# Kernel tuning notes

Hardware: AMD Instinct MI355X
Metric: run time of the kernel (lower is better)

## Reference

```python
import jax, jax.numpy as jnp
import numpy as np

B, N, DIM = 8, 2048, 512
HEADS, DIM_HEAD = 8, 64
INNER = HEADS * DIM_HEAD  # 512
SCALE = DIM_HEAD ** -0.5
NEG = -1e9


def setup_inputs() -> dict:
    key = jax.random.key(0)
    ks = jax.random.split(key, 7)
    x = jax.random.normal(ks[0], (B, N, DIM), dtype=jnp.float32)
    adj = jax.random.uniform(ks[1], (B, N, N), dtype=jnp.float32)
    att_mask = jax.random.randint(ks[2], (B, 1, N, N), 0, 2).astype(jnp.bool_)
    W_gcn = jax.random.normal(ks[3], (DIM, DIM), dtype=jnp.float32) * (DIM ** -0.5)
    W_qkv = jax.random.normal(ks[4], (DIM, 3 * INNER), dtype=jnp.float32) * (DIM ** -0.5)
    W_out = jax.random.normal(ks[5], (INNER + DIM, DIM), dtype=jnp.float32) * ((INNER + DIM) ** -0.5)
    b_out = jax.random.normal(ks[6], (DIM,), dtype=jnp.float32) * 0.01
    return {"x": x, "adj": adj, "att_mask": att_mask,
            "W_gcn": W_gcn, "W_qkv": W_qkv, "W_out": W_out, "b_out": b_out}


def reference(x, adj, att_mask, W_gcn, W_qkv, W_out, b_out):
    # GCN branch: adj @ (x W_gcn)  -> [b, n, dim]
    gcn = jnp.einsum('bnj,bjd->bnd', adj, x @ W_gcn)

    # Attention branch
    qkv = x @ W_qkv                                  # [b, n, 3*inner]
    q, k, v = jnp.split(qkv, 3, axis=-1)
    split_heads = lambda t: t.reshape(B, N, HEADS, DIM_HEAD).transpose(0, 2, 1, 3)
    q, k, v = split_heads(q), split_heads(k), split_heads(v)  # [b, h, n, d]

    dots = jnp.einsum('bhid,bhjd->bhij', q, k) * SCALE        # [b, h, n, n]
    dots = jnp.where(att_mask, NEG, dots)
    attn = jax.nn.softmax(dots, axis=-1)
    att_out = jnp.einsum('bhij,bhjd->bhid', attn, v)          # [b, h, n, d]
    att_out = att_out.transpose(0, 2, 1, 3).reshape(B, N, INNER)

    out = jnp.concatenate([att_out, gcn], axis=-1)            # [b, n, inner+dim]
    return out @ W_out + b_out                                # [b, n, dim]
```

## Files before the change

### kernel.cpp

```cpp
#include <hip/hip_runtime.h>
#include <stdint.h>

#define DEVFN __device__ __forceinline__

typedef __attribute__((ext_vector_type(8))) short short8;
typedef __attribute__((ext_vector_type(4))) short short4v;
typedef __attribute__((ext_vector_type(4))) float floatx4;
typedef __attribute__((ext_vector_type(16))) float floatx16;
typedef __attribute__((ext_vector_type(4))) float vfloat4;
typedef __attribute__((ext_vector_type(2))) unsigned int uint2v;
typedef __attribute__((ext_vector_type(4))) unsigned int uint4v;

#define MFMA_BF16(a,b,c) __builtin_amdgcn_mfma_f32_16x16x32_bf16((a),(b),(c),0,0,0)
#define MFMA32_BF16(a,b,c) __builtin_amdgcn_mfma_f32_32x32x16_bf16((a),(b),(c),0,0,0)
#define GL2LDS(g,l) __builtin_amdgcn_global_load_lds((const __attribute__((address_space(1))) void*)(g), (__attribute__((address_space(3))) void*)(l), 16, 0, 0)

DEVFN unsigned short f2bf(float f){
  unsigned u = __float_as_uint(f);
  u = (u + 0x7fffu + ((u >> 16) & 1u)) >> 16;
  return (unsigned short)u;
}

DEVFN unsigned cvtpk_bf16(float lo, float hi){
  unsigned r;
  asm("v_cvt_pk_bf16_f32 %0, %1, %2" : "=v"(r) : "v"(lo), "v"(hi));
  return r;
}

__global__ void detect_kernel(const unsigned char* m, unsigned int* flag){
  if (threadIdx.x == 0) *flag = 0u;
  __syncthreads();
  int any = 0;
  for (int i = threadIdx.x; i < 4096; i += 256)
    if ((i & 3) != 0 && m[i]) any = 1;
  if (any) atomicOr(flag, 1u);
}

__global__ void prep_kernel(const float* __restrict__ x, const float* __restrict__ wg,
                            const float* __restrict__ wq, const float* __restrict__ wo,
                            const void* __restrict__ mask, const unsigned* __restrict__ flag,
                            const float* __restrict__ adj,
                            unsigned short* __restrict__ xbf, unsigned short* __restrict__ wcat,
                            unsigned short* __restrict__ woutT, unsigned* __restrict__ mp,
                            unsigned short* __restrict__ adjb)
{
  int bid = blockIdx.x, tid = threadIdx.x;
  if (bid < 8192) {
    int i = (bid*256 + tid)*4;
    vfloat4 v = *(const vfloat4*)&x[i];
    short4v c; c[0]=(short)f2bf(v[0]); c[1]=(short)f2bf(v[1]); c[2]=(short)f2bf(v[2]); c[3]=(short)f2bf(v[3]);
    *(short4v*)&xbf[i] = c;
  } else if (bid < 8192 + 4096) {
    int i = (bid - 8192)*256 + tid;
    int k = i & 511, c = i >> 9;
    float v = (c < 512) ? wg[k*512 + c] : wq[k*1536 + (c - 512)];
    if (c >= 512 && c < 1024) v *= 0.18033688f;
    wcat[c*512 + k] = (unsigned short)f2bf(v);
  } else if (bid < 8192 + 4096 + 2048) {
    int i = (bid - 12288)*256 + tid;
    int k = i & 1023, n2 = i >> 10;
    woutT[n2*1024 + k] = (unsigned short)f2bf(wo[k*512 + n2]);
  } else if (bid < 145408) {
    int j = bid - 14336;
    int e = j*256 + tid;
    int v;
    if (*flag) v = ((const unsigned char*)mask)[e];
    else       v = ((const int*)mask)[e];
    unsigned long long ball = __ballot(v != 0);
    int base = e & ~63;
    int lane = tid & 63;
    if (lane == 0)  mp[(base >> 5) + 0] = (unsigned)(ball & 0xffffffffull);
    if (lane == 32) mp[(base >> 5) + 1] = (unsigned)(ball >> 32);
  } else {
    int i = ((bid - 145408)*256 + tid)*4;
    vfloat4 v = *(const vfloat4*)&adj[i];
    short4v c; c[0]=(short)f2bf(v[0]); c[1]=(short)f2bf(v[1]); c[2]=(short)f2bf(v[2]); c[3]=(short)f2bf(v[3]);
    *(short4v*)&adjb[i] = c;
  }
}

DEVFN void gemm_kloop_bf16(const unsigned short* Ag, int lda,
                           const unsigned short* Bg, int ldb, int K,
                           short* As, short* Bs, int w, int l,
                           floatx4 (&acc)[4][4])
{
  const int wr = (w >> 1)*64, wc = (w & 1)*64;
  for (int k0 = 0; k0 < K; k0 += 32) {
    __syncthreads();
#pragma unroll
    for (int i = 0; i < 2; i++) {
      int id = (w*2 + i)*64 + l;
      int row = id >> 2, part = id & 3;
      GL2LDS(Ag + row*lda + k0 + part*8, As + (w*2 + i)*512);
      GL2LDS(Bg + row*ldb + k0 + part*8, Bs + (w*2 + i)*512);
    }
    __syncthreads();
    short8 af[4], bfr[4];
#pragma unroll
    for (int t = 0; t < 4; t++) {
      af[t]  = *(const short8*)&As[(wr + t*16 + (l & 15))*32 + ((l >> 4) << 3)];
      bfr[t] = *(const short8*)&Bs[(wc + t*16 + (l & 15))*32 + ((l >> 4) << 3)];
    }
#pragma unroll
    for (int a2 = 0; a2 < 4; a2++)
#pragma unroll
      for (int b2 = 0; b2 < 4; b2++)
        acc[a2][b2] = MFMA_BF16(af[a2], bfr[b2], acc[a2][b2]);
  }
}

__global__ __launch_bounds__(256, 2)
void gemm_ab_kernel(const unsigned short* __restrict__ xbf, const unsigned short* __restrict__ wcat,
                    unsigned short* __restrict__ xgT, unsigned short* __restrict__ Qo,
                    unsigned short* __restrict__ Ko, unsigned short* __restrict__ VTo)
{
  __shared__ short lds[16384];
  int tid = threadIdx.x, w = tid >> 6, l = tid & 63;
  int bid = blockIdx.x;
  int xcd = bid & 7, slot = bid >> 3;
  int p  = xcd + ((slot >> 4) << 3);
  int nt = slot & 15;
  int rows0 = p*128, cols0 = nt*128;

  floatx4 acc[4][4];
  const floatx4 zf = {0.f, 0.f, 0.f, 0.f};
#pragma unroll
  for (int a2 = 0; a2 < 4; a2++)
#pragma unroll
    for (int b2 = 0; b2 < 4; b2++) acc[a2][b2] = zf;

  gemm_kloop_bf16(xbf + rows0*512, 512, wcat + cols0*512, 512, 512,
                  lds, lds + 4096, w, l, acc);
  __syncthreads();

  int wr = (w >> 1)*64, wc = (w & 1)*64;
  int b = p >> 4;
  int n0 = (p & 15)*128 + wr;
  int gc0 = cols0 + wc;

  if (nt < 4 || nt >= 12) {
    short* T = lds + w*4096;
#pragma unroll
    for (int mi = 0; mi < 4; mi++)
#pragma unroll
      for (int bi = 0; bi < 4; bi++)
#pragma unroll
        for (int r = 0; r < 4; r++) {
          int rl = mi*16 + ((l >> 4) << 2) + r;
          int cl = bi*16 + (l & 15);
          T[cl*64 + ((((rl >> 3) ^ (cl & 7))) << 3) + (rl & 7)] = (short)f2bf(acc[mi][bi][r]);
        }
#pragma unroll
    for (int i = 0; i < 8; i++) {
      int chunk = i*64 + l;
      int c = chunk >> 3, s = chunk & 7;
      short8 v = *(const short8*)&T[c*64 + ((s ^ (c & 7)) << 3)];
      int rowstart = n0 + s*8;
      if (nt < 4) {
        int d = gc0 + c;
        *(short8*)&xgT[(b*512 + d)*2048 + rowstart] = v;
      } else {
        int vc = gc0 + c - 1536;
        int hh = vc >> 6, dd = vc & 63;
        *(short8*)&VTo[((b*8 + hh)*64 + dd)*2048 + rowstart] = v;
      }
    }
  } else {
    unsigned short* dst = (nt < 8) ? Qo : Ko;
    int cbase = gc0 - ((nt < 8) ? 512 : 1024);
    int hh = cbase >> 6;
#pragma unroll
    for (int mi = 0; mi < 4; mi++)
#pragma unroll
      for (int bi = 0; bi < 4; bi++)
#pragma unroll
        for (int r = 0; r < 4; r++) {
          int rowg = n0 + mi*16 + ((l >> 4) << 2) + r;
          int dd = bi*16 + (l & 15);
          dst[((b*8 + hh)*2048 + rowg)*64 + dd] = (unsigned short)f2bf(acc[mi][bi][r]);
        }
  }
}

__global__ __launch_bounds__(256, 2)
void gemm_c_bf16_kernel(const unsigned short* __restrict__ adjb, const unsigned short* __restrict__ xgT,
                        unsigned short* __restrict__ cat)
{
  __shared__ short lds[8192];
  int tid = threadIdx.x, w = tid >> 6, l = tid & 63;
  int bid = blockIdx.x;
  int xcd = bid & 7, slot = bid >> 3;
  int p  = xcd + ((slot >> 2) << 3);
  int nt = slot & 3;
  int b = p >> 4, mt = p & 15;
  int rows0 = mt*128, cols0 = nt*128;

  floatx4 acc[4][4];
  const floatx4 zf = {0.f, 0.f, 0.f, 0.f};
#pragma unroll
  for (int a2 = 0; a2 < 4; a2++)
#pragma unroll
    for (int b2 = 0; b2 < 4; b2++) acc[a2][b2] = zf;

  gemm_kloop_bf16(adjb + (size_t)b*2048*2048 + (size_t)rows0*2048, 2048,
                  xgT + (b*512 + cols0)*2048, 2048, 2048,
                  lds, lds + 4096, w, l, acc);

  int wr = (w >> 1)*64, wc = (w & 1)*64;
#pragma unroll
  for (int mi = 0; mi < 4; mi++)
#pragma unroll
    for (int bi = 0; bi < 4; bi++)
#pragma unroll
      for (int r = 0; r < 4; r++) {
        int rowg = b*2048 + rows0 + wr + mi*16 + ((l >> 4) << 2) + r;
        int col  = 512 + cols0 + wc + bi*16 + (l & 15);
        cat[rowg*1024 + col] = (unsigned short)f2bf(acc[mi][bi][r]);
      }
}

__global__ __launch_bounds__(256, 2)
void gemm_c_f32_kernel(const float* __restrict__ adj, const unsigned short* __restrict__ xgT,
                       unsigned short* __restrict__ cat)
{
  __shared__ short lds[8192];
  int tid = threadIdx.x, w = tid >> 6, l = tid & 63;
  int bid = blockIdx.x;
  int xcd = bid & 7, slot = bid >> 3;
  int p  = xcd + ((slot >> 2) << 3);
  int nt = slot & 3;
  int b = p >> 4, mt = p & 15;
  int rows0 = mt*128, cols0 = nt*128;
  const float* Ag = adj + (size_t)b*2048*2048 + (size_t)rows0*2048;
  const unsigned short* Bg = xgT + (b*512 + cols0)*2048;

  floatx4 acc[4][4];
  const floatx4 zf = {0.f, 0.f, 0.f, 0.f};
#pragma unroll
  for (int a2 = 0; a2 < 4; a2++)
#pragma unroll
    for (int b2 = 0; b2 < 4; b2++) acc[a2][b2] = zf;

  const int wr = (w >> 1)*64, wc = (w & 1)*64;
  for (int k0 = 0; k0 < 2048; k0 += 32) {
    __syncthreads();
#pragma unroll
    for (int i = 0; i < 4; i++) {
      int id = (w*4 + i)*64 + l;
      int row = id >> 3, part = id & 7;
      vfloat4 v = *(const vfloat4*)&Ag[row*2048 + k0 + part*4];
      short4v c4; c4[0]=(short)f2bf(v[0]); c4[1]=(short)f2bf(v[1]); c4[2]=(short)f2bf(v[2]); c4[3]=(short)f2bf(v[3]);
      *(short4v*)&lds[row*32 + part*4] = c4;
    }
#pragma unroll
    for (int i = 0; i < 2; i++) {
      int id = (w*2 + i)*64 + l;
      int row = id >> 2, part = id & 3;
      GL2LDS(Bg + row*2048 + k0 + part*8, lds + 4096 + (w*2 + i)*512);
    }
    __syncthreads();
    short8 af[4], bfr[4];
#pragma unroll
    for (int t = 0; t < 4; t++) {
      af[t]  = *(const short8*)&lds[(wr + t*16 + (l & 15))*32 + ((l >> 4) << 3)];
      bfr[t] = *(const short8*)&lds[4096 + (wc + t*16 + (l & 15))*32 + ((l >> 4) << 3)];
    }
#pragma unroll
    for (int a2 = 0; a2 < 4; a2++)
#pragma unroll
      for (int b2 = 0; b2 < 4; b2++)
        acc[a2][b2] = MFMA_BF16(af[a2], bfr[b2], acc[a2][b2]);
  }

#pragma unroll
  for (int mi = 0; mi < 4; mi++)
#pragma unroll
    for (int bi = 0; bi < 4; bi++)
#pragma unroll
      for (int r = 0; r < 4; r++) {
        int rowg = b*2048 + rows0 + wr + mi*16 + ((l >> 4) << 2) + r;
        int col  = 512 + cols0 + wc + bi*16 + (l & 15);
        cat[rowg*1024 + col] = (unsigned short)f2bf(acc[mi][bi][r]);
      }
}

DEVFN void attn_stage(const unsigned short* KB, const unsigned short* VB,
                      short* Ks, short* Vs, int kn0, int w, int l)
{
#pragma unroll
  for (int i = 0; i < 2; i++) {
    int id = (w*2 + i)*64 + l;
    int row = id >> 3, sl = id & 7;
    int sp = sl ^ (row & 7) ^ (((row >> 3) & 3) << 1);
    GL2LDS(KB + (kn0 + row)*64 + sp*8, Ks + (w*2 + i)*512);
    GL2LDS(VB + row*2048 + kn0 + sp*8, Vs + (w*2 + i)*512);
  }
}

__global__ __launch_bounds__(256, 4)
void attn_kernel(const unsigned short* __restrict__ Q, const unsigned short* __restrict__ Kb,
                 const unsigned short* __restrict__ VT, const unsigned* __restrict__ mp,
                 unsigned short* __restrict__ cat)
{
  __shared__ short lds[16384];
  int tid = threadIdx.x, w = tid >> 6, l = tid & 63;
  int c5 = l & 31, h = l >> 5;
  int hv = h*4;

  int bid = blockIdx.x;
  int xcd = bid & 7, slot = bid >> 3;
  int bh = xcd + ((slot >> 4) << 3);
  int qt = slot & 15;
  int b = bh >> 3, hd = bh & 7;
  int qw = qt*128 + w*32;

  const unsigned short* Qb = Q  + (size_t)bh*2048*64;
  const unsigned short* KB = Kb + (size_t)bh*2048*64;
  const unsigned short* VB = VT + (size_t)bh*64*2048;
  const unsigned* mrow = mp + b*2048*64 + (qw + c5)*64;

  short8 qf[4];
#pragma unroll
  for (int dk = 0; dk < 4; dk++)
    qf[dk] = *(const short8*)&Qb[(qw + c5)*64 + dk*16 + h*8];

  floatx16 oacc0, oacc1, nacc;
  const floatx16 zf16 = {0.f,0.f,0.f,0.f,0.f,0.f,0.f,0.f,0.f,0.f,0.f,0.f,0.f,0.f,0.f,0.f};
  oacc0 = zf16; oacc1 = zf16; nacc = zf16;

  const short8 ones8 = {(short)0x3F80,(short)0x3F80,(short)0x3F80,(short)0x3F80,
                        (short)0x3F80,(short)0x3F80,(short)0x3F80,(short)0x3F80};

  attn_stage(KB, VB, lds, lds + 8192, 0, w, l);
  uint2v wd = *(const uint2v*)&mrow[0];
  asm volatile("s_waitcnt vmcnt(0)" ::: "memory");
  __builtin_amdgcn_s_barrier();
  asm volatile("" ::: "memory");

  for (int kt = 0; kt < 32; kt++) {
    int cur = kt & 1;
    short* Ks = lds + cur*4096;
    short* Vs = lds + 8192 + cur*4096;

    if (kt < 31)
      attn_stage(KB, VB, lds + (cur ^ 1)*4096, lds + 8192 + (cur ^ 1)*4096, kt*64 + 64, w, l);

    uint2v wdn = wd;
    if (kt < 31) wdn = *(const uint2v*)&mrow[(kt + 1)*2];

#pragma unroll
    for (int kb = 0; kb < 2; kb++) {
      floatx16 sacc = zf16;
      __builtin_amdgcn_s_setprio(1);
#pragma unroll
      for (int dk = 0; dk < 4; dk++) {
        int row = kb*32 + c5;
        int sl = dk*2 + h;
        int sw = sl ^ (row & 7) ^ (((row >> 3) & 3) << 1);
        short8 kf = *(const short8*)&Ks[row*64 + (sw << 3)];
        sacc = MFMA32_BF16(kf, qf[dk], sacc);
      }
      __builtin_amdgcn_s_setprio(0);

      unsigned keep = ~((kb ? wd.y : wd.x) >> hv);
      float ps[16];
#pragma unroll
      for (int t = 0; t < 16; t++) {
        int pos = (t >> 2)*8 + (t & 3);
        int keepm = (int)(keep << (31 - pos)) >> 31;
        float p = exp2f(sacc[t]);
        ps[t] = __uint_as_float(__float_as_uint(p) & (unsigned)keepm);
      }
      unsigned pk[4][2];
#pragma unroll
      for (int s = 0; s < 4; s++) {
        pk[s][0] = cvtpk_bf16(ps[s*4 + 0], ps[s*4 + 1]);
        pk[s][1] = cvtpk_bf16(ps[s*4 + 2], ps[s*4 + 3]);
      }

#pragma unroll
      for (int ksl = 0; ksl < 2; ksl++) {
        uint2v s0 = __builtin_amdgcn_permlane32_swap(pk[2*ksl][0], pk[2*ksl + 1][0], false, false);
        uint2v s1 = __builtin_amdgcn_permlane32_swap(pk[2*ksl][1], pk[2*ksl + 1][1], false, false);
        uint4v fu;
        fu[0] = s0.x;
        fu[1] = s1.x;
        fu[2] = s0.y;
        fu[3] = s1.y;
        short8 pfrag = *(short8*)&fu;

        __builtin_amdgcn_s_setprio(1);
#pragma unroll
        for (int db = 0; db < 2; db++) {
          int row = db*32 + c5;
          int sl = kb*4 + ksl*2 + h;
          int sw = sl ^ (row & 7) ^ (((row >> 3) & 3) << 1);
          short8 vf = *(const short8*)&Vs[row*64 + (sw << 3)];
          if (db == 0) oacc0 = MFMA32_BF16(pfrag, vf, oacc0);
          else         oacc1 = MFMA32_BF16(pfrag, vf, oacc1);
        }
        nacc = MFMA32_BF16(pfrag, ones8, nacc);
        __builtin_amdgcn_s_setprio(0);
      }
    }
    wd = wdn;

    asm volatile("s_waitcnt vmcnt(0)" ::: "memory");
    __builtin_amdgcn_s_barrier();
    asm volatile("" ::: "memory");
  }

#pragma unroll
  for (int t = 0; t < 16; t++) {
    float iv = 1.0f / nacc[t];
    int qrow = qw + (t & 3) + 8*(t >> 2) + hv;
    unsigned short* orow = &cat[(b*2048 + qrow)*1024 + hd*64];
    orow[c5]      = (unsigned short)f2bf(oacc0[t] * iv);
    orow[32 + c5] = (unsigned short)f2bf(oacc1[t] * iv);
  }
}

__global__ __launch_bounds__(256, 2)
void gemm_d_kernel(const unsigned short* __restrict__ cat, const unsigned short* __restrict__ woutT,
                   const float* __restrict__ bout, float* __restrict__ out)
{
  __shared__ short lds[8192];
  int tid = threadIdx.x, w = tid >> 6, l = tid & 63;
  int bid = blockIdx.x;
  int xcd = bid & 7, slot = bid >> 3;
  int p  = xcd + ((slot >> 2) << 3);
  int nt = slot & 3;
  int rows0 = p*128, cols0 = nt*128;

  floatx4 acc[4][4];
  const floatx4 zf = {0.f, 0.f, 0.f, 0.f};
#pragma unroll
  for (int a2 = 0; a2 < 4; a2++)
#pragma unroll
    for (int b2 = 0; b2 < 4; b2++) acc[a2][b2] = zf;

  gemm_kloop_bf16(cat + (size_t)rows0*1024, 1024, woutT + cols0*1024, 1024, 1024,
                  lds, lds + 4096, w, l, acc);

  int wr = (w >> 1)*64, wc = (w & 1)*64;
#pragma unroll
  for (int bi = 0; bi < 4; bi++) {
    int col = cols0 + wc + bi*16 + (l & 15);
    float bias = bout[col];
#pragma unroll
    for (int mi = 0; mi < 4; mi++)
#pragma unroll
      for (int r = 0; r < 4; r++) {
        int rowg = rows0 + wr + mi*16 + ((l >> 4) << 2) + r;
        out[rowg*512 + col] = acc[mi][bi][r] + bias;
      }
  }
}

extern "C" void kernel_launch(void* const* d_in, const int* in_sizes, int n_in,
                              void* d_out, int out_size, void* d_ws, size_t ws_size,
                              hipStream_t stream)
{
  (void)in_sizes; (void)n_in; (void)out_size;
  const float* x   = (const float*)d_in[0];
  const float* adj = (const float*)d_in[1];
  const void*  msk = d_in[2];
  const float* wg  = (const float*)d_in[3];
  const float* wq  = (const float*)d_in[4];
  const float* wo  = (const float*)d_in[5];
  const float* bo  = (const float*)d_in[6];
  float* out = (float*)d_out;
  char* ws = (char*)d_ws;

  unsigned short* xbf   = (unsigned short*)(ws + 0);
  unsigned short* wcat  = (unsigned short*)(ws + 16777216);
  unsigned short* woutT = (unsigned short*)(ws + 18874368);
  unsigned short* xgT   = (unsigned short*)(ws + 19922944);
  unsigned short* Qb    = (unsigned short*)(ws + 36700160);
  unsigned short* Kb    = (unsigned short*)(ws + 53477376);
  unsigned short* VTb   = (unsigned short*)(ws + 70254592);
  unsigned short* cat   = (unsigned short*)(ws + 87031808);
  unsigned*       mp    = (unsigned*)(ws + 120586240);
  unsigned*       flag  = (unsigned*)(ws + 124780544);
  unsigned short* adjb  = (unsigned short*)(ws + 124780608);

  const int use_adjb = (ws_size >= (size_t)124780608 + 67108864) ? 1 : 0;

  detect_kernel<<<1, 256, 0, stream>>>((const unsigned char*)msk, flag);
  prep_kernel<<<use_adjb ? 178176 : 145408, 256, 0, stream>>>(
      x, wg, wq, wo, msk, flag, adj, xbf, wcat, woutT, mp, adjb);
  gemm_ab_kernel<<<2048, 256, 0, stream>>>(xbf, wcat, xgT, Qb, Kb, VTb);
  if (use_adjb)
    gemm_c_bf16_kernel<<<512, 256, 0, stream>>>(adjb, xgT, cat);
  else
    gemm_c_f32_kernel<<<512, 256, 0, stream>>>(adj, xgT, cat);
  attn_kernel<<<1024, 256, 0, stream>>>(Qb, Kb, VTb, mp, cat);
  gemm_d_kernel<<<512, 256, 0, stream>>>(cat, woutT, bo, out);
}
```

Baseline: 388.9 us.

## Fuse adjacency GEMM and attention into one launch with interleaved block roles

New measurement: 377.7 us. 1.03x faster.

```diff
diff --git a/kernel.cpp b/kernel.cpp
--- a/kernel.cpp
+++ b/kernel.cpp
@@ -183,43 +183,6 @@
 }
 
 __global__ __launch_bounds__(256, 2)
-void gemm_c_bf16_kernel(const unsigned short* __restrict__ adjb, const unsigned short* __restrict__ xgT,
-                        unsigned short* __restrict__ cat)
-{
-  __shared__ short lds[8192];
-  int tid = threadIdx.x, w = tid >> 6, l = tid & 63;
-  int bid = blockIdx.x;
-  int xcd = bid & 7, slot = bid >> 3;
-  int p  = xcd + ((slot >> 2) << 3);
-  int nt = slot & 3;
-  int b = p >> 4, mt = p & 15;
-  int rows0 = mt*128, cols0 = nt*128;
-
-  floatx4 acc[4][4];
-  const floatx4 zf = {0.f, 0.f, 0.f, 0.f};
-#pragma unroll
-  for (int a2 = 0; a2 < 4; a2++)
-#pragma unroll
-    for (int b2 = 0; b2 < 4; b2++) acc[a2][b2] = zf;
-
-  gemm_kloop_bf16(adjb + (size_t)b*2048*2048 + (size_t)rows0*2048, 2048,
-                  xgT + (b*512 + cols0)*2048, 2048, 2048,
-                  lds, lds + 4096, w, l, acc);
-
-  int wr = (w >> 1)*64, wc = (w & 1)*64;
-#pragma unroll
-  for (int mi = 0; mi < 4; mi++)
-#pragma unroll
-    for (int bi = 0; bi < 4; bi++)
-#pragma unroll
-      for (int r = 0; r < 4; r++) {
-        int rowg = b*2048 + rows0 + wr + mi*16 + ((l >> 4) << 2) + r;
-        int col  = 512 + cols0 + wc + bi*16 + (l & 15);
-        cat[rowg*1024 + col] = (unsigned short)f2bf(acc[mi][bi][r]);
-      }
-}
-
-__global__ __launch_bounds__(256, 2)
 void gemm_c_f32_kernel(const float* __restrict__ adj, const unsigned short* __restrict__ xgT,
                        unsigned short* __restrict__ cat)
 {
@@ -297,18 +260,16 @@
   }
 }
 
-__global__ __launch_bounds__(256, 4)
-void attn_kernel(const unsigned short* __restrict__ Q, const unsigned short* __restrict__ Kb,
-                 const unsigned short* __restrict__ VT, const unsigned* __restrict__ mp,
-                 unsigned short* __restrict__ cat)
-{
-  __shared__ short lds[16384];
+DEVFN void attn_body(int abid, short* lds,
+                     const unsigned short* __restrict__ Q, const unsigned short* __restrict__ Kb,
+                     const unsigned short* __restrict__ VT, const unsigned* __restrict__ mp,
+                     unsigned short* __restrict__ cat)
+{
   int tid = threadIdx.x, w = tid >> 6, l = tid & 63;
   int c5 = l & 31, h = l >> 5;
   int hv = h*4;
 
-  int bid = blockIdx.x;
-  int xcd = bid & 7, slot = bid >> 3;
+  int xcd = abid & 7, slot = abid >> 3;
   int bh = xcd + ((slot >> 4) << 3);
   int qt = slot & 15;
   int b = bh >> 3, hd = bh & 7;
@@ -367,7 +328,7 @@
 #pragma unroll
       for (int t = 0; t < 16; t++) {
         int pos = (t >> 2)*8 + (t & 3);
-        int keepm = (int)(keep << (31 - pos)) >> 31;
+        int keepm = __builtin_amdgcn_sbfe((int)keep, pos, 1);
         float p = exp2f(sacc[t]);
         ps[t] = __uint_as_float(__float_as_uint(p) & (unsigned)keepm);
       }
@@ -417,6 +378,61 @@
     unsigned short* orow = &cat[(b*2048 + qrow)*1024 + hd*64];
     orow[c5]      = (unsigned short)f2bf(oacc0[t] * iv);
     orow[32 + c5] = (unsigned short)f2bf(oacc1[t] * iv);
+  }
+}
+
+__global__ __launch_bounds__(256, 4)
+void attn_kernel(const unsigned short* __restrict__ Q, const unsigned short* __restrict__ Kb,
+                 const unsigned short* __restrict__ VT, const unsigned* __restrict__ mp,
+                 unsigned short* __restrict__ cat)
+{
+  __shared__ short lds[16384];
+  attn_body(blockIdx.x, lds, Q, Kb, VT, mp, cat);
+}
+
+__global__ __launch_bounds__(256, 3)
+void fused_ca_kernel(const unsigned short* __restrict__ adjb, const unsigned short* __restrict__ xgT,
+                     const unsigned short* __restrict__ Q, const unsigned short* __restrict__ Kb,
+                     const unsigned short* __restrict__ VT, const unsigned* __restrict__ mp,
+                     unsigned short* __restrict__ cat)
+{
+  __shared__ short lds[16384];
+  int bid = blockIdx.x;
+  int r3 = bid % 3;
+  if (r3 == 2) {
+    int cbid = bid / 3;
+    int tid = threadIdx.x, w = tid >> 6, l = tid & 63;
+    int xcd = cbid & 7, slot = cbid >> 3;
+    int p  = xcd + ((slot >> 2) << 3);
+    int nt = slot & 3;
+    int b = p >> 4, mt = p & 15;
+    int rows0 = mt*128, cols0 = nt*128;
+
+    floatx4 acc[4][4];
+    const floatx4 zf = {0.f, 0.f, 0.f, 0.f};
+#pragma unroll
+    for (int a2 = 0; a2 < 4; a2++)
+#pragma unroll
+      for (int b2 = 0; b2 < 4; b2++) acc[a2][b2] = zf;
+
+    gemm_kloop_bf16(adjb + (size_t)b*2048*2048 + (size_t)rows0*2048, 2048,
+                    xgT + (b*512 + cols0)*2048, 2048, 2048,
+                    lds, lds + 4096, w, l, acc);
+
+    int wr = (w >> 1)*64, wc = (w & 1)*64;
+#pragma unroll
+    for (int mi = 0; mi < 4; mi++)
+#pragma unroll
+      for (int bi = 0; bi < 4; bi++)
+#pragma unroll
+        for (int r = 0; r < 4; r++) {
+          int rowg = b*2048 + rows0 + wr + mi*16 + ((l >> 4) << 2) + r;
+          int col  = 512 + cols0 + wc + bi*16 + (l & 15);
+          cat[rowg*1024 + col] = (unsigned short)f2bf(acc[mi][bi][r]);
+        }
+  } else {
+    int abid = (bid / 3)*2 + r3;
+    attn_body(abid, lds, Q, Kb, VT, mp, cat);
   }
 }
 
@@ -490,10 +506,11 @@
   prep_kernel<<<use_adjb ? 178176 : 145408, 256, 0, stream>>>(
       x, wg, wq, wo, msk, flag, adj, xbf, wcat, woutT, mp, adjb);
   gemm_ab_kernel<<<2048, 256, 0, stream>>>(xbf, wcat, xgT, Qb, Kb, VTb);
-  if (use_adjb)
-    gemm_c_bf16_kernel<<<512, 256, 0, stream>>>(adjb, xgT, cat);
-  else
+  if (use_adjb) {
+    fused_ca_kernel<<<1536, 256, 0, stream>>>(adjb, xgT, Qb, Kb, VTb, mp, cat);
+  } else {
     gemm_c_f32_kernel<<<512, 256, 0, stream>>>(adj, xgT, cat);
-  attn_kernel<<<1024, 256, 0, stream>>>(Qb, Kb, VTb, mp, cat);
+    attn_kernel<<<1024, 256, 0, stream>>>(Qb, Kb, VTb, mp, cat);
+  }
   gemm_d_kernel<<<512, 256, 0, stream>>>(cat, woutT, bo, out);
 }
```
